# Optimization experiments

Hardware: AMD Instinct MI355X
Metric: run time of the kernel (lower is better)

## Reference

```python
import math
import jax, jax.numpy as jnp
import numpy as np

N, H, E, K = 8192, 2048, 8, 2
CF = 1.25


def setup_inputs() -> dict:
    key = jax.random.key(0)
    ks = jax.random.split(key, 5)
    s1 = 1.0 / math.sqrt(H)
    s2 = 1.0 / math.sqrt(2 * H)
    return {
        "tokens": jax.random.normal(ks[0], (N, H), jnp.float32),
        "Wr": jax.random.normal(ks[1], (E, H), jnp.float32) * s1,   # router: logits = x @ Wr.T + br
        "br": jnp.zeros((E,), jnp.float32),
        "W1": jax.random.normal(ks[2], (E, H, 2 * H), jnp.float32) * s1,
        "b1": jnp.zeros((E, 2 * H), jnp.float32),
        "W2": jax.random.normal(ks[3], (E, 2 * H, H), jnp.float32) * s2,
        "b2": jnp.zeros((E, H), jnp.float32),
    }


def reference(tokens, Wr, br, W1, b1, W2, b2):
    n = tokens.shape[0]
    cap = max(1, math.ceil(CF * n / E))  # per-expert capacity (static)

    # --- router + top-k ---
    logits = tokens @ Wr.T + br                         # [N, E]
    scores, expert_ids = jax.lax.top_k(logits, K)       # [N, K]
    probs = jax.nn.softmax(scores, axis=-1)

    # --- flatten dispatches and sort by expert (stable, like the torch code) ---
    flat_e = expert_ids.reshape(-1)                     # [N*K]
    flat_t = jnp.repeat(jnp.arange(n), K)               # [N*K]
    flat_s = probs.reshape(-1).astype(tokens.dtype)     # [N*K]
    order = jnp.argsort(flat_e)                         # jnp.argsort is stable
    se, st, ss = flat_e[order], flat_t[order], flat_s[order]

    # --- capacity-limited gather: fixed [E, cap] index grid ---
    seg_start = jnp.searchsorted(se, jnp.arange(E))     # [E] first slot of each expert segment
    counts = jnp.bincount(se, length=E)                 # [E] tokens routed to each expert
    slot = jnp.arange(cap)
    idx = jnp.clip(seg_start[:, None] + slot[None, :], 0, n * K - 1)  # [E, cap]
    valid = slot[None, :] < jnp.minimum(counts, cap)[:, None]          # [E, cap]
    tok_idx = st[idx]                                   # [E, cap] source token ids
    w = jnp.where(valid, ss[idx], 0.0)[..., None]       # [E, cap, 1] combine weights (0 => dropped)

    # --- grouped per-expert FFN (GEMM over [E, cap, H]) ---
    x = tokens[tok_idx]                                 # [E, cap, H]
    h = jax.nn.gelu(jnp.einsum('ech,ehf->ecf', x, W1) + b1[:, None, :], approximate=False)
    y = jnp.einsum('ecf,efh->ech', h, W2) + b2[:, None, :]

    # --- weighted scatter-add combine ---
    out = jnp.zeros_like(tokens).at[tok_idx.reshape(-1)].add((y * w).reshape(-1, tokens.shape[-1]))
    return out
```

## Files before the change

### kernel.cpp

```cpp
#include <hip/hip_runtime.h>
#include <hip/hip_bf16.h>
#include <math.h>

#define NTOK 8192
#define HDIM 2048
#define NEXP 8
#define TOPK 2
#define CAP  1280
#define FF   4096
#define BK   64

typedef float  f32x4  __attribute__((ext_vector_type(4)));
typedef __bf16 bf16x8 __attribute__((ext_vector_type(8)));

typedef __attribute__((address_space(1))) const unsigned int gas_u32;
typedef __attribute__((address_space(3))) unsigned int las_u32;

__device__ __forceinline__ void gload16(const void* g, void* l) {
    __builtin_amdgcn_global_load_lds((gas_u32*)g, (las_u32*)l, 16, 0, 0);
}

__device__ __forceinline__ ushort f2bf(float f) {
    union { float f; unsigned u; } c; c.f = f;
    unsigned u = c.u;
    unsigned r = (u + 0x7FFFu + ((u >> 16) & 1u)) >> 16;
    return (ushort)r;
}
__device__ __forceinline__ float bf2f(ushort h) {
    union { unsigned u; float f; } c; c.u = ((unsigned)h) << 16;
    return c.f;
}

__global__ void k_convert(const float* __restrict__ src, ushort* __restrict__ dst) {
    int i = (blockIdx.x * 256 + threadIdx.x) * 8;
    float4 a = *(const float4*)(src + i);
    float4 b = *(const float4*)(src + i + 4);
    uint4 o;
    o.x = (unsigned)f2bf(a.x) | ((unsigned)f2bf(a.y) << 16);
    o.y = (unsigned)f2bf(a.z) | ((unsigned)f2bf(a.w) << 16);
    o.z = (unsigned)f2bf(b.x) | ((unsigned)f2bf(b.y) << 16);
    o.w = (unsigned)f2bf(b.z) | ((unsigned)f2bf(b.w) << 16);
    *(uint4*)(dst + i) = o;
}

__global__ void k_router(const float* __restrict__ tokens, const float* __restrict__ Wr,
                         const float* __restrict__ br, int* __restrict__ eids,
                         float* __restrict__ probs) {
    int wave = threadIdx.x >> 6, lane = threadIdx.x & 63;
    int t = blockIdx.x * 4 + wave;
    const float* tp = tokens + (size_t)t * HDIM;
    double acc[NEXP];
    #pragma unroll
    for (int e = 0; e < NEXP; ++e) acc[e] = 0.0;
    for (int j = 0; j < HDIM / 64; ++j) {
        float x = tp[j * 64 + lane];
        #pragma unroll
        for (int e = 0; e < NEXP; ++e)
            acc[e] += (double)x * (double)Wr[e * HDIM + j * 64 + lane];
    }
    #pragma unroll
    for (int e = 0; e < NEXP; ++e) {
        #pragma unroll
        for (int off = 32; off; off >>= 1) acc[e] += __shfl_xor(acc[e], off, 64);
    }
    if (lane == 0) {
        float lg[NEXP];
        #pragma unroll
        for (int e = 0; e < NEXP; ++e) lg[e] = (float)acc[e] + br[e];
        int e0 = 0; float s0 = lg[0];
        #pragma unroll
        for (int e = 1; e < NEXP; ++e) if (lg[e] > s0) { s0 = lg[e]; e0 = e; }
        int e1 = -1; float s1 = -1e30f;
        #pragma unroll
        for (int e = 0; e < NEXP; ++e) if (e != e0 && lg[e] > s1) { s1 = lg[e]; e1 = e; }
        float ex = expf(s1 - s0);
        float den = 1.f + ex;
        eids[t * 2] = e0; eids[t * 2 + 1] = e1;
        probs[t * 2] = 1.f / den; probs[t * 2 + 1] = ex / den;
    }
}

__global__ void k_assign(const int* __restrict__ eids, int* __restrict__ tok_map,
                         int* __restrict__ dest) {
    __shared__ int cnt[64][NEXP];
    int l = threadIdx.x;
    for (int i = l; i < NEXP * CAP; i += 64) tok_map[i] = 0;
    int c[NEXP];
    #pragma unroll
    for (int e = 0; e < NEXP; ++e) c[e] = 0;
    const int base = l * 256;
    for (int i = 0; i < 256; ++i) {
        int ee = eids[base + i];
        #pragma unroll
        for (int e = 0; e < NEXP; ++e) c[e] += (ee == e);
    }
    #pragma unroll
    for (int e = 0; e < NEXP; ++e) cnt[l][e] = c[e];
    __syncthreads();
    if (l < NEXP) {
        int run = 0;
        for (int b = 0; b < 64; ++b) { int v = cnt[b][l]; cnt[b][l] = run; run += v; }
    }
    __syncthreads();
    int off[NEXP];
    #pragma unroll
    for (int e = 0; e < NEXP; ++e) off[e] = cnt[l][e];
    for (int i = 0; i < 256; ++i) {
        int d = base + i;
        int ee = eids[d];
        int r = -1;
        #pragma unroll
        for (int e = 0; e < NEXP; ++e) { bool m = (ee == e); if (m) r = off[e]; off[e] += m; }
        if (r < CAP) { tok_map[ee * CAP + r] = d >> 1; dest[d] = ee * CAP + r; }
        else dest[d] = -1;
    }
}

__global__ __launch_bounds__(256) void k_transpose(const float* __restrict__ src,
                                                   ushort* __restrict__ dst,
                                                   int Kd, int Nd) {
    __shared__ float tl[64][65];
    int e = blockIdx.z;
    int k0 = blockIdx.x * 64, n0 = blockIdx.y * 64;
    const float* s = src + (size_t)e * Kd * Nd;
    ushort* d = dst + (size_t)e * Kd * Nd;
    int tid = threadIdx.x;
    #pragma unroll
    for (int i = 0; i < 4; ++i) {
        int flat = (i * 256 + tid) * 4;
        int kk = flat >> 6, nn = flat & 63;
        float4 v = *(const float4*)(s + (size_t)(k0 + kk) * Nd + n0 + nn);
        tl[kk][nn] = v.x; tl[kk][nn + 1] = v.y; tl[kk][nn + 2] = v.z; tl[kk][nn + 3] = v.w;
    }
    __syncthreads();
    #pragma unroll
    for (int g = 0; g < 4; ++g) {
        int flat = g * 1024 + tid * 4;
        int nn = flat >> 6, kk = flat & 63;
        uint2 o;
        o.x = (unsigned)f2bf(tl[kk][nn])     | ((unsigned)f2bf(tl[kk + 1][nn]) << 16);
        o.y = (unsigned)f2bf(tl[kk + 2][nn]) | ((unsigned)f2bf(tl[kk + 3][nn]) << 16);
        *(uint2*)(d + (size_t)(n0 + nn) * Kd + k0 + kk) = o;
    }
}

#define SCHED0() __builtin_amdgcn_sched_barrier(0)
#define VMC0()   do { asm volatile("s_waitcnt vmcnt(0)" ::: "memory"); } while (0)

template<bool DOGELU, bool GATHER>
__global__ __launch_bounds__(256) void k_gemm(const ushort* __restrict__ A,
                                              const int* __restrict__ tmap,
                                              const ushort* __restrict__ B,
                                              const float* __restrict__ bias,
                                              ushort* __restrict__ C,
                                              int Kd, int Nd) {
    __shared__ __attribute__((aligned(128))) char lds[65536];
    const int tid  = threadIdx.x;
    const int lane = tid & 63;
    const int wave = tid >> 6;
    const int wr = wave >> 1, wc = wave & 1;
    const int e = blockIdx.z;
    const int bm0 = blockIdx.y * 128, bn0 = blockIdx.x * 128;

    const ushort* Be = B + (size_t)e * (size_t)Nd * Kd;
    const int rbase = tid >> 3;
    const int kc = (((tid & 7) ^ (rbase & 7))) * 8;
    const ushort* pa[4]; const ushort* pb[4];
    #pragma unroll
    for (int r = 0; r < 4; ++r) {
        int gr = r * 32 + rbase;
        int arow = GATHER ? tmap[e * CAP + bm0 + gr] : (e * CAP + bm0 + gr);
        pa[r] = A  + (size_t)arow * Kd + kc;
        pb[r] = Be + (size_t)(bn0 + gr) * Kd + kc;
    }

    auto STAGE = [&](int buf, int kt) {
        char* d = lds + buf * 32768;
        #pragma unroll
        for (int r = 0; r < 4; ++r)
            gload16(pa[r] + kt * BK, d + r * 4096 + tid * 16);
        #pragma unroll
        for (int r = 0; r < 4; ++r)
            gload16(pb[r] + kt * BK, d + 16384 + r * 4096 + tid * 16);
    };

    const int fr = lane & 15, kq = lane >> 4;
    int offA[4][2], offB[4][2];
    #pragma unroll
    for (int m = 0; m < 4; ++m) {
        int row = wr * 64 + m * 16 + fr;
        #pragma unroll
        for (int ks = 0; ks < 2; ++ks)
            offA[m][ks] = row * 128 + (((ks * 4 + kq) ^ (row & 7)) * 16);
    }
    #pragma unroll
    for (int n = 0; n < 4; ++n) {
        int row = wc * 64 + n * 16 + fr;
        #pragma unroll
        for (int ks = 0; ks < 2; ++ks)
            offB[n][ks] = 16384 + row * 128 + (((ks * 4 + kq) ^ (row & 7)) * 16);
    }

    f32x4 acc[4][4] = {};
    const int nt = Kd / BK;

    STAGE(0, 0);
    VMC0();
    __builtin_amdgcn_s_barrier();
    for (int t = 0; t < nt; ++t) {
        if (t + 1 < nt) STAGE((t + 1) & 1, t + 1);
        SCHED0();
        const char* rb = lds + (t & 1) * 32768;
        bf16x8 af[4][2], bf[4][2];
        #pragma unroll
        for (int m = 0; m < 4; ++m)
            #pragma unroll
            for (int ks = 0; ks < 2; ++ks)
                af[m][ks] = *(const bf16x8*)(rb + offA[m][ks]);
        #pragma unroll
        for (int n = 0; n < 4; ++n)
            #pragma unroll
            for (int ks = 0; ks < 2; ++ks)
                bf[n][ks] = *(const bf16x8*)(rb + offB[n][ks]);
        #pragma unroll
        for (int ks = 0; ks < 2; ++ks)
            #pragma unroll
            for (int m = 0; m < 4; ++m)
                #pragma unroll
                for (int n = 0; n < 4; ++n)
                    acc[m][n] = __builtin_amdgcn_mfma_f32_16x16x32_bf16(af[m][ks], bf[n][ks],
                                                                        acc[m][n], 0, 0, 0);
        VMC0();
        __builtin_amdgcn_s_barrier();
    }

    const float* be = bias + e * Nd;
    ushort* Ce = C + (size_t)e * CAP * Nd;
    const int rl = (lane >> 4) * 4, cl = lane & 15;
    #pragma unroll
    for (int mi = 0; mi < 4; ++mi) {
        #pragma unroll
        for (int ni = 0; ni < 4; ++ni) {
            #pragma unroll
            for (int r = 0; r < 4; ++r) {
                int gr = bm0 + wr * 64 + mi * 16 + rl + r;
                int gc = bn0 + wc * 64 + ni * 16 + cl;
                float v = acc[mi][ni][r] + be[gc];
                if (DOGELU) v = 0.5f * v * (1.f + erff(v * 0.70710678118654752f));
                Ce[(size_t)gr * Nd + gc] = f2bf(v);
            }
        }
    }
}

__global__ void k_combine(const ushort* __restrict__ Y, const int* __restrict__ dest,
                          const float* __restrict__ probs, float* __restrict__ out) {
    int t = blockIdx.x;
    int h0 = threadIdx.x * 8;
    int d0 = dest[t * 2], d1 = dest[t * 2 + 1];
    float p0 = d0 >= 0 ? probs[t * 2] : 0.f;
    float p1 = d1 >= 0 ? probs[t * 2 + 1] : 0.f;
    int r0 = d0 >= 0 ? d0 : 0, r1 = d1 >= 0 ? d1 : 0;
    uint4 a = *(const uint4*)(Y + (size_t)r0 * HDIM + h0);
    uint4 b = *(const uint4*)(Y + (size_t)r1 * HDIM + h0);
    float4 o0, o1;
    o0.x = p0 * bf2f(a.x & 0xffff) + p1 * bf2f(b.x & 0xffff);
    o0.y = p0 * bf2f(a.x >> 16)    + p1 * bf2f(b.x >> 16);
    o0.z = p0 * bf2f(a.y & 0xffff) + p1 * bf2f(b.y & 0xffff);
    o0.w = p0 * bf2f(a.y >> 16)    + p1 * bf2f(b.y >> 16);
    o1.x = p0 * bf2f(a.z & 0xffff) + p1 * bf2f(b.z & 0xffff);
    o1.y = p0 * bf2f(a.z >> 16)    + p1 * bf2f(b.z >> 16);
    o1.z = p0 * bf2f(a.w & 0xffff) + p1 * bf2f(b.w & 0xffff);
    o1.w = p0 * bf2f(a.w >> 16)    + p1 * bf2f(b.w >> 16);
    float* op = out + (size_t)t * HDIM + h0;
    *(float4*)op = o0;
    *(float4*)(op + 4) = o1;
}

extern "C" void kernel_launch(void* const* d_in, const int* in_sizes, int n_in,
                              void* d_out, int out_size, void* d_ws, size_t ws_size,
                              hipStream_t stream) {
    const float* tokens = (const float*)d_in[0];
    const float* Wr     = (const float*)d_in[1];
    const float* br     = (const float*)d_in[2];
    const float* W1     = (const float*)d_in[3];
    const float* b1     = (const float*)d_in[4];
    const float* W2     = (const float*)d_in[5];
    const float* b2     = (const float*)d_in[6];
    float* out = (float*)d_out;
    char* ws = (char*)d_ws;

    int*    eids    = (int*)(ws);
    float*  probs   = (float*)(ws + 65536);
    int*    tok_map = (int*)(ws + 131072);
    int*    dest    = (int*)(ws + 172032);
    size_t off = 1u << 20;
    ushort* TbY = (ushort*)(ws + off);
    off += 41943040;
    ushort* Hm  = (ushort*)(ws + off);
    off += 83886080;
    ushort* WT  = (ushort*)(ws + off);
    (void)in_sizes; (void)n_in; (void)out_size; (void)ws_size;

    k_convert<<<dim3(NTOK * HDIM / 2048), 256, 0, stream>>>(tokens, TbY);
    k_router<<<dim3(NTOK / 4), 256, 0, stream>>>(tokens, Wr, br, eids, probs);
    k_assign<<<dim3(1), 64, 0, stream>>>(eids, tok_map, dest);
    k_transpose<<<dim3(HDIM / 64, FF / 64, NEXP), 256, 0, stream>>>(W1, WT, HDIM, FF);
    k_gemm<true, true><<<dim3(FF / 128, CAP / 128, NEXP), 256, 0, stream>>>(
        TbY, tok_map, WT, b1, Hm, HDIM, FF);
    k_transpose<<<dim3(FF / 64, HDIM / 64, NEXP), 256, 0, stream>>>(W2, WT, FF, HDIM);
    k_gemm<false, false><<<dim3(HDIM / 128, CAP / 128, NEXP), 256, 0, stream>>>(
        Hm, nullptr, WT, b2, TbY, FF, HDIM);
    k_combine<<<dim3(NTOK), 256, 0, stream>>>(TbY, dest, probs, out);
}
```

Baseline: 732.0 us.

## Enlarge grouped GEMM tiles to 320x256 with 8 waves per block

```diff
diff --git a/kernel.cpp b/kernel.cpp
--- a/kernel.cpp
+++ b/kernel.cpp
@@ -9,6 +9,8 @@
 #define CAP  1280
 #define FF   4096
 #define BK   64
+#define BM   320
+#define BN   256
 
 typedef float  f32x4  __attribute__((ext_vector_type(4)));
 typedef __bf16 bf16x8 __attribute__((ext_vector_type(8)));
@@ -148,60 +150,62 @@
 #define VMC0()   do { asm volatile("s_waitcnt vmcnt(0)" ::: "memory"); } while (0)
 
 template<bool DOGELU, bool GATHER>
-__global__ __launch_bounds__(256) void k_gemm(const ushort* __restrict__ A,
-                                              const int* __restrict__ tmap,
-                                              const ushort* __restrict__ B,
-                                              const float* __restrict__ bias,
-                                              ushort* __restrict__ C,
-                                              int Kd, int Nd) {
-    __shared__ __attribute__((aligned(128))) char lds[65536];
+__global__ __launch_bounds__(512, 1) void k_gemm(const ushort* __restrict__ A,
+                                                 const int* __restrict__ tmap,
+                                                 const ushort* __restrict__ B,
+                                                 const float* __restrict__ bias,
+                                                 ushort* __restrict__ C,
+                                                 int Kd, int Nd) {
+    __shared__ __attribute__((aligned(128))) char lds[147456];
     const int tid  = threadIdx.x;
     const int lane = tid & 63;
     const int wave = tid >> 6;
     const int wr = wave >> 1, wc = wave & 1;
     const int e = blockIdx.z;
-    const int bm0 = blockIdx.y * 128, bn0 = blockIdx.x * 128;
+    const int bm0 = blockIdx.y * BM, bn0 = blockIdx.x * BN;
 
     const ushort* Be = B + (size_t)e * (size_t)Nd * Kd;
     const int rbase = tid >> 3;
-    const int kc = (((tid & 7) ^ (rbase & 7))) * 8;
-    const ushort* pa[4]; const ushort* pb[4];
-    #pragma unroll
-    for (int r = 0; r < 4; ++r) {
-        int gr = r * 32 + rbase;
+    const int kc = ((tid & 7) ^ (rbase & 7)) * 8;
+    const ushort* pa[5]; const ushort* pb[4];
+    #pragma unroll
+    for (int q = 0; q < 5; ++q) {
+        int gr = q * 64 + rbase;
         int arow = GATHER ? tmap[e * CAP + bm0 + gr] : (e * CAP + bm0 + gr);
-        pa[r] = A  + (size_t)arow * Kd + kc;
-        pb[r] = Be + (size_t)(bn0 + gr) * Kd + kc;
-    }
+        pa[q] = A + (size_t)arow * Kd + kc;
+    }
+    #pragma unroll
+    for (int q = 0; q < 4; ++q)
+        pb[q] = Be + (size_t)(bn0 + q * 64 + rbase) * Kd + kc;
 
     auto STAGE = [&](int buf, int kt) {
-        char* d = lds + buf * 32768;
-        #pragma unroll
-        for (int r = 0; r < 4; ++r)
-            gload16(pa[r] + kt * BK, d + r * 4096 + tid * 16);
-        #pragma unroll
-        for (int r = 0; r < 4; ++r)
-            gload16(pb[r] + kt * BK, d + 16384 + r * 4096 + tid * 16);
+        char* d = lds + buf * 73728;
+        #pragma unroll
+        for (int q = 0; q < 5; ++q)
+            gload16(pa[q] + kt * BK, d + q * 8192 + tid * 16);
+        #pragma unroll
+        for (int q = 0; q < 4; ++q)
+            gload16(pb[q] + kt * BK, d + 40960 + q * 8192 + tid * 16);
     };
 
     const int fr = lane & 15, kq = lane >> 4;
-    int offA[4][2], offB[4][2];
-    #pragma unroll
-    for (int m = 0; m < 4; ++m) {
-        int row = wr * 64 + m * 16 + fr;
+    int offA[5][2], offB[8][2];
+    #pragma unroll
+    for (int m = 0; m < 5; ++m) {
+        int row = wr * 80 + m * 16 + fr;
         #pragma unroll
         for (int ks = 0; ks < 2; ++ks)
             offA[m][ks] = row * 128 + (((ks * 4 + kq) ^ (row & 7)) * 16);
     }
     #pragma unroll
-    for (int n = 0; n < 4; ++n) {
-        int row = wc * 64 + n * 16 + fr;
+    for (int n = 0; n < 8; ++n) {
+        int row = wc * 128 + n * 16 + fr;
         #pragma unroll
         for (int ks = 0; ks < 2; ++ks)
-            offB[n][ks] = 16384 + row * 128 + (((ks * 4 + kq) ^ (row & 7)) * 16);
-    }
-
-    f32x4 acc[4][4] = {};
+            offB[n][ks] = 40960 + row * 128 + (((ks * 4 + kq) ^ (row & 7)) * 16);
+    }
+
+    f32x4 acc[5][8] = {};
     const int nt = Kd / BK;
 
     STAGE(0, 0);
@@ -210,24 +214,24 @@
     for (int t = 0; t < nt; ++t) {
         if (t + 1 < nt) STAGE((t + 1) & 1, t + 1);
         SCHED0();
-        const char* rb = lds + (t & 1) * 32768;
-        bf16x8 af[4][2], bf[4][2];
-        #pragma unroll
-        for (int m = 0; m < 4; ++m)
+        const char* rb = lds + (t & 1) * 73728;
+        bf16x8 af[5][2], bf[8][2];
+        #pragma unroll
+        for (int m = 0; m < 5; ++m)
             #pragma unroll
             for (int ks = 0; ks < 2; ++ks)
                 af[m][ks] = *(const bf16x8*)(rb + offA[m][ks]);
         #pragma unroll
-        for (int n = 0; n < 4; ++n)
+        for (int n = 0; n < 8; ++n)
             #pragma unroll
             for (int ks = 0; ks < 2; ++ks)
                 bf[n][ks] = *(const bf16x8*)(rb + offB[n][ks]);
         #pragma unroll
         for (int ks = 0; ks < 2; ++ks)
             #pragma unroll
-            for (int m = 0; m < 4; ++m)
+            for (int m = 0; m < 5; ++m)
                 #pragma unroll
-                for (int n = 0; n < 4; ++n)
+                for (int n = 0; n < 8; ++n)
                     acc[m][n] = __builtin_amdgcn_mfma_f32_16x16x32_bf16(af[m][ks], bf[n][ks],
                                                                         acc[m][n], 0, 0, 0);
         VMC0();
@@ -238,14 +242,15 @@
     ushort* Ce = C + (size_t)e * CAP * Nd;
     const int rl = (lane >> 4) * 4, cl = lane & 15;
     #pragma unroll
-    for (int mi = 0; mi < 4; ++mi) {
-        #pragma unroll
-        for (int ni = 0; ni < 4; ++ni) {
+    for (int ni = 0; ni < 8; ++ni) {
+        int gc = bn0 + wc * 128 + ni * 16 + cl;
+        float bv = be[gc];
+        #pragma unroll
+        for (int mi = 0; mi < 5; ++mi) {
             #pragma unroll
             for (int r = 0; r < 4; ++r) {
-                int gr = bm0 + wr * 64 + mi * 16 + rl + r;
-                int gc = bn0 + wc * 64 + ni * 16 + cl;
-                float v = acc[mi][ni][r] + be[gc];
+                int gr = bm0 + wr * 80 + mi * 16 + rl + r;
+                float v = acc[mi][ni][r] + bv;
                 if (DOGELU) v = 0.5f * v * (1.f + erff(v * 0.70710678118654752f));
                 Ce[(size_t)gr * Nd + gc] = f2bf(v);
             }
@@ -306,10 +311,10 @@
     k_router<<<dim3(NTOK / 4), 256, 0, stream>>>(tokens, Wr, br, eids, probs);
     k_assign<<<dim3(1), 64, 0, stream>>>(eids, tok_map, dest);
     k_transpose<<<dim3(HDIM / 64, FF / 64, NEXP), 256, 0, stream>>>(W1, WT, HDIM, FF);
-    k_gemm<true, true><<<dim3(FF / 128, CAP / 128, NEXP), 256, 0, stream>>>(
+    k_gemm<true, true><<<dim3(FF / BN, CAP / BM, NEXP), 512, 0, stream>>>(
         TbY, tok_map, WT, b1, Hm, HDIM, FF);
     k_transpose<<<dim3(FF / 64, HDIM / 64, NEXP), 256, 0, stream>>>(W2, WT, FF, HDIM);
-    k_gemm<false, false><<<dim3(HDIM / 128, CAP / 128, NEXP), 256, 0, stream>>>(
+    k_gemm<false, false><<<dim3(HDIM / BN, CAP / BM, NEXP), 512, 0, stream>>>(
         Hm, nullptr, WT, b2, TbY, FF, HDIM);
     k_combine<<<dim3(NTOK), 256, 0, stream>>>(TbY, dest, probs, out);
 }
```

Result: slower. 747.7 us (+2.1%).
